# Kernel optimization log

Hardware: AMD Instinct MI355X
Metric: run time of the kernel (lower is better)

Reference implementation:

```python
import jax, jax.numpy as jnp
import numpy as np

B, S, D_IN, D = 8, 8192, 512, 512  # batch, seq_len, input_dim, dim (dim_inner = dim since expansion=1.0)


def log_g(x):
    # log-space version of g(x) = relu(x)+0.5 for x>=0, sigmoid(x) for x<0
    return jnp.where(x >= 0, jnp.log(jax.nn.relu(x) + 0.5), -jax.nn.softplus(-x))


def heinsen_scan_log(log_coeffs, log_values):
    # parallel linear-recurrence solve in log space
    a_star = jnp.cumsum(log_coeffs, axis=1)                       # [B, S+1, D]
    log_h = a_star + jax.lax.cumlogsumexp(log_values - a_star, axis=1)
    return jnp.exp(log_h)


def setup_inputs() -> dict:
    key = jax.random.key(0)
    k1, k2, k3 = jax.random.split(key, 3)
    x = jax.random.normal(k1, (B, S, D_IN), dtype=jnp.float32)
    prev_hidden = jax.random.normal(k2, (B, D), dtype=jnp.float32)
    W = jax.random.normal(k3, (D_IN, 2 * D), dtype=jnp.float32) / np.sqrt(D_IN)
    return {"x": x, "prev_hidden": prev_hidden, "W": W}


def reference(x, prev_hidden, W):
    seq_len = x.shape[1]
    hidden_gate = jnp.einsum('bsi,id->bsd', x, W)                 # [B, S, 2D]
    hidden, gate = jnp.split(hidden_gate, 2, axis=-1)             # [B, S, D] each
    log_coeffs = -jax.nn.softplus(gate)                           # log(1 - z)
    log_z = -jax.nn.softplus(-gate)                               # log(z)
    log_values = log_z + log_g(hidden)                            # log(z * h_tilde)
    # prepend previous hidden state as step 0 of the recurrence
    log_values = jnp.concatenate([log_g(prev_hidden)[:, None, :], log_values], axis=1)  # [B, S+1, D]
    log_coeffs = jnp.pad(log_coeffs, ((0, 0), (1, 0), (0, 0)))     # [B, S+1, D]
    h = heinsen_scan_log(log_coeffs, log_values)                  # [B, S+1, D]
    out = h[:, -seq_len:]                                         # [B, S, D]
    return out  # to_out is identity since expansion_factor == 1.0
```

## Files before the change

### kernel.cpp

```cpp
#include <hip/hip_runtime.h>
#include <stdint.h>

#define Bb   8
#define Ss   8192
#define DIN  512
#define Dd   512
#define M_TOT (Bb * Ss)
#define NC   64
#define CL   128

static const size_t CV_OFF  = 0;
static const size_t XS_OFF  = 134217728ull;
static const size_t WT_OFF  = XS_OFF + 67108864ull;
static const size_t AG_OFF  = WT_OFF + 1048576ull;
static const size_t HIN_OFF = AG_OFF + 2097152ull;
static const size_t WS_NEED = HIN_OFF + 1048576ull;

typedef short  short8 __attribute__((ext_vector_type(8)));
typedef float  f32x4  __attribute__((ext_vector_type(4)));

__device__ __forceinline__ unsigned short bf16_rne(float f) {
  uint32_t u = __float_as_uint(f);
  u += 0x7fffu + ((u >> 16) & 1u);
  return (unsigned short)(u >> 16);
}

__device__ __forceinline__ void gload16(const unsigned short* g, void* l) {
  __builtin_amdgcn_global_load_lds(
      (const __attribute__((address_space(1))) uint32_t*)g,
      (__attribute__((address_space(3))) uint32_t*)l, 16, 0, 0);
}

__global__ void k_prep(const float* __restrict__ x, const float* __restrict__ W,
                       unsigned short* __restrict__ xs, unsigned short* __restrict__ wt) {
  const int bx = blockIdx.x;
  if (bx < 4096) {
    const size_t n4 = (size_t)M_TOT * DIN / 4;
    for (size_t i = (size_t)bx * 256 + threadIdx.x; i < n4; i += (size_t)4096 * 256) {
      float4 v = ((const float4*)x)[i];
      size_t e = i * 4;
      size_t r = e >> 9;
      int    k = (int)(e & 511);
      ushort4 hi;
      unsigned short* hp = (unsigned short*)&hi;
      hp[0] = bf16_rne(v.x); hp[1] = bf16_rne(v.y);
      hp[2] = bf16_rne(v.z); hp[3] = bf16_rne(v.w);
      *(ushort4*)(xs + r * 512 + k) = hi;
    }
  } else {
    const int t0 = (bx - 4096) * 256 + threadIdx.x;
    for (int i = t0; i < 1024 * 512; i += 131072) {
      int n = i >> 9;
      int k = i & 511;
      int t = n >> 5, u = n & 31;
      int j = 16 * t + (u & 15) + ((u & 16) ? 512 : 0);
      wt[i] = bf16_rne(W[(size_t)k * 1024 + j]);
    }
  }
}

__global__ void __launch_bounds__(256) k_gemm(const unsigned short* __restrict__ xs,
                                              const unsigned short* __restrict__ wt,
                                              uint32_t* __restrict__ cvu,
                                              float2* __restrict__ agg) {
  __shared__ __align__(16) unsigned short As[2][128 * 32];
  __shared__ __align__(16) unsigned short Bsh[2][128 * 32];
  __shared__ float aggC[2][2][2][16];
  __shared__ float aggV[2][2][2][16];

  const int tid  = threadIdx.x;
  const int lane = tid & 63;
  const int wave = tid >> 6;
  const int wr = wave >> 1, wc = wave & 1;

  const int bid = blockIdx.x;
  const int xcd = bid & 7;
  const int j8  = bid >> 3;
  const int mb  = xcd * 64 + (j8 >> 3);
  const int nb  = j8 & 7;
  const int m0 = mb * 128, n0 = nb * 128;

  f32x4 acc[4][4] = {};

  const int trow = tid >> 2;
  const int tks  = 8 * ((tid & 3) ^ ((tid >> 3) & 3));
  const size_t aoff0 = (size_t)(m0 + trow) * 512 + tks;
  const size_t aoff1 = aoff0 + (size_t)64 * 512;
  const size_t boff0 = (size_t)(n0 + trow) * 512 + tks;
  const size_t boff1 = boff0 + (size_t)64 * 512;

  const int ra = (lane & 15) * 32 + 8 * ((lane >> 4) ^ ((lane >> 1) & 3));

#define STAGE(bf, k0) { \
    char* la = (char*)As  + (bf) * 8192 + wave * 1024; \
    char* lb = (char*)Bsh + (bf) * 8192 + wave * 1024; \
    gload16(xs + aoff0 + (k0), la); \
    gload16(xs + aoff1 + (k0), la + 4096); \
    gload16(wt + boff0 + (k0), lb); \
    gload16(wt + boff1 + (k0), lb + 4096); }

#define COMPUTE(bf) { \
    const unsigned short* Ab = &As[bf][0]; \
    const unsigned short* Bb2 = &Bsh[bf][0]; \
    short8 af[4], bfr[4]; \
    _Pragma("unroll") for (int m = 0; m < 4; ++m) \
      af[m] = *(const short8*)(Ab + (wr * 64 + 16 * m) * 32 + ra); \
    _Pragma("unroll") for (int n = 0; n < 4; ++n) \
      bfr[n] = *(const short8*)(Bb2 + (wc * 64 + 16 * n) * 32 + ra); \
    _Pragma("unroll") for (int m = 0; m < 4; ++m) \
      _Pragma("unroll") for (int n = 0; n < 4; ++n) \
        acc[m][n] = __builtin_amdgcn_mfma_f32_16x16x32_bf16(af[m], bfr[n], acc[m][n], 0, 0, 0); }

  STAGE(0, 0);
  __syncthreads();
  int buf = 0;
  for (int kt = 0; kt < 15; ++kt) {
    STAGE(buf ^ 1, (kt + 1) * 32);
    COMPUTE(buf);
    __syncthreads();
    buf ^= 1;
  }
  COMPUTE(buf);

  const int q     = lane >> 4;
  const int rbase = m0 + wr * 64 + (q << 2);
  const int dbase = nb * 64 + wc * 32 + (lane & 15);

  float CW[2] = {1.f, 1.f};
  float VW[2] = {0.f, 0.f};

#pragma unroll
  for (int m = 0; m < 4; ++m) {
#pragma unroll
    for (int t = 0; t < 2; ++t) {
      float cseg = 1.f, vseg = 0.f;
#pragma unroll
      for (int j = 0; j < 4; ++j) {
        float hid = acc[m][2 * t][j];
        float gat = acc[m][2 * t + 1][j];
        float eg = __expf(gat);
        float c  = 1.f / (1.f + eg);
        float z  = 1.f - c;
        float gv = (hid >= 0.f) ? (hid + 0.5f) : (1.f / (1.f + __expf(-hid)));
        float v  = z * gv;
        int R = rbase + 16 * m + j;
        int d = dbase + 16 * t;
        cvu[(size_t)R * 512 + d] =
            (uint32_t)bf16_rne(c) | ((uint32_t)bf16_rne(v) << 16);
        vseg = fmaf(c, vseg, v);
        cseg *= c;
      }
      {
        float Cp = __shfl_xor(cseg, 16);
        float Vp = __shfl_xor(vseg, 16);
        if (q & 1) { vseg = fmaf(cseg, Vp, vseg); cseg = Cp * cseg; }
        else       { vseg = fmaf(Cp, vseg, Vp);   cseg = cseg * Cp; }
        Cp = __shfl_xor(cseg, 32);
        Vp = __shfl_xor(vseg, 32);
        if (q & 2) { vseg = fmaf(cseg, Vp, vseg); cseg = Cp * cseg; }
        else       { vseg = fmaf(Cp, vseg, Vp);   cseg = cseg * Cp; }
      }
      VW[t] = fmaf(cseg, VW[t], vseg);
      CW[t] *= cseg;
    }
  }

  if (lane < 16) {
#pragma unroll
    for (int t = 0; t < 2; ++t) {
      aggC[wr][wc][t][lane] = CW[t];
      aggV[wr][wc][t][lane] = VW[t];
    }
  }
  __syncthreads();
  if (wr == 0 && lane < 16) {
#pragma unroll
    for (int t = 0; t < 2; ++t) {
      float C1 = aggC[1][wc][t][lane];
      float V1 = aggV[1][wc][t][lane];
      int d = nb * 64 + wc * 32 + t * 16 + lane;
      agg[(size_t)mb * 512 + d] = make_float2(CW[t] * C1, fmaf(C1, VW[t], V1));
    }
  }
}

__global__ void k_chain(const float* __restrict__ prev, const float2* __restrict__ agg,
                        float* __restrict__ hin) {
  const int b = blockIdx.x >> 1;
  const int d = (blockIdx.x & 1) * 256 + threadIdx.x;
  float p = prev[b * 512 + d];
  float h = (p >= 0.f) ? (p + 0.5f) : (1.f / (1.f + __expf(-p)));
  float2 a[NC];
#pragma unroll
  for (int k = 0; k < NC; ++k)
    a[k] = agg[((size_t)(b * NC + k)) * 512 + d];
#pragma unroll
  for (int k = 0; k < NC; ++k) {
    hin[((size_t)(b * NC + k)) * 512 + d] = h;
    h = fmaf(a[k].x, h, a[k].y);
  }
}

__global__ void k_scan_out(const uint32_t* __restrict__ cvu, const float* __restrict__ hin,
                           float* __restrict__ out) {
  const int bid = blockIdx.x;
  const int chunk = bid & 63;
  const int b = bid >> 6;
  const int d0 = threadIdx.x * 2;
  float2 h2 = *(const float2*)(hin + ((size_t)(b * NC + chunk)) * 512 + d0);
  const size_t base = ((size_t)(b * Ss + chunk * CL)) * 512 + d0;
#pragma unroll 8
  for (int i = 0; i < CL; ++i) {
    uint2 t = *(const uint2*)(cvu + base + (size_t)i * 512);
    float c0 = __uint_as_float(t.x << 16);
    float v0 = __uint_as_float(t.x & 0xFFFF0000u);
    float c1 = __uint_as_float(t.y << 16);
    float v1 = __uint_as_float(t.y & 0xFFFF0000u);
    h2.x = fmaf(c0, h2.x, v0);
    h2.y = fmaf(c1, h2.y, v1);
    *(float2*)(out + base + (size_t)i * 512) = h2;
  }
}

extern "C" void kernel_launch(void* const* d_in, const int* in_sizes, int n_in,
                              void* d_out, int out_size, void* d_ws, size_t ws_size,
                              hipStream_t stream) {
  if (ws_size < WS_NEED) return;

  const float* x    = (const float*)d_in[0];
  const float* prev = (const float*)d_in[1];
  const float* W    = (const float*)d_in[2];
  float* out = (float*)d_out;
  char* ws = (char*)d_ws;

  uint32_t*       cvu = (uint32_t*)(ws + CV_OFF);
  unsigned short* xs  = (unsigned short*)(ws + XS_OFF);
  unsigned short* wt  = (unsigned short*)(ws + WT_OFF);
  float2*         agg = (float2*)(ws + AG_OFF);
  float*          hin = (float*)(ws + HIN_OFF);

  k_prep<<<dim3(4608), dim3(256), 0, stream>>>(x, W, xs, wt);
  k_gemm<<<dim3(4096), dim3(256), 0, stream>>>(xs, wt, cvu, agg);
  k_chain<<<dim3(16), dim3(256), 0, stream>>>(prev, agg, hin);
  k_scan_out<<<dim3(512), dim3(256), 0, stream>>>(cvu, hin, out);
}
```

Before: 377.1 us.

## Enlarge GEMM M-tile to 256 rows and coalesce the W transpose reads

The fused GEMM+gate kernel now computes a 256x128 output tile per block, with each wave holding 8x4 MFMA accumulators, which halves the grid and doubles A-operand reuse per B load. Each wave writes its own 128-row chunk aggregate directly, so the shared-memory cross-wave combine and its barrier are gone. The chunk indexing stays consistent with the 64 chunks of 128 rows used by the chain and scan kernels. The W conversion in the prep kernel now reads W contiguously and scatters the writes instead of gathering strided reads. The risks are more register pressure (launch bounds set to 2 blocks), lower occupancy, and fewer blocks to balance across CUs.

```diff
diff --git a/kernel.cpp b/kernel.cpp
--- a/kernel.cpp
+++ b/kernel.cpp
@@ -49,24 +49,23 @@
     }
   } else {
     const int t0 = (bx - 4096) * 256 + threadIdx.x;
-    for (int i = t0; i < 1024 * 512; i += 131072) {
-      int n = i >> 9;
-      int k = i & 511;
-      int t = n >> 5, u = n & 31;
-      int j = 16 * t + (u & 15) + ((u & 16) ? 512 : 0);
-      wt[i] = bf16_rne(W[(size_t)k * 1024 + j]);
-    }
-  }
-}
-
-__global__ void __launch_bounds__(256) k_gemm(const unsigned short* __restrict__ xs,
-                                              const unsigned short* __restrict__ wt,
-                                              uint32_t* __restrict__ cvu,
-                                              float2* __restrict__ agg) {
-  __shared__ __align__(16) unsigned short As[2][128 * 32];
+    for (int i = t0; i < 512 * 1024; i += 131072) {
+      int k = i >> 10;
+      int j = i & 1023;
+      float w = W[i];
+      int n = (j < 512) ? (32 * (j >> 4) + (j & 15))
+                        : (32 * ((j - 512) >> 4) + 16 + ((j - 512) & 15));
+      wt[n * 512 + k] = bf16_rne(w);
+    }
+  }
+}
+
+__global__ void __launch_bounds__(256, 2) k_gemm(const unsigned short* __restrict__ xs,
+                                                 const unsigned short* __restrict__ wt,
+                                                 uint32_t* __restrict__ cvu,
+                                                 float2* __restrict__ agg) {
+  __shared__ __align__(16) unsigned short As[2][256 * 32];
   __shared__ __align__(16) unsigned short Bsh[2][128 * 32];
-  __shared__ float aggC[2][2][2][16];
-  __shared__ float aggV[2][2][2][16];
 
   const int tid  = threadIdx.x;
   const int lane = tid & 63;
@@ -76,38 +75,42 @@
   const int bid = blockIdx.x;
   const int xcd = bid & 7;
   const int j8  = bid >> 3;
-  const int mb  = xcd * 64 + (j8 >> 3);
+  const int mb  = xcd * 32 + (j8 >> 3);
   const int nb  = j8 & 7;
-  const int m0 = mb * 128, n0 = nb * 128;
-
-  f32x4 acc[4][4] = {};
+  const int m0 = mb * 256, n0 = nb * 128;
+
+  f32x4 acc[8][4] = {};
 
   const int trow = tid >> 2;
   const int tks  = 8 * ((tid & 3) ^ ((tid >> 3) & 3));
   const size_t aoff0 = (size_t)(m0 + trow) * 512 + tks;
   const size_t aoff1 = aoff0 + (size_t)64 * 512;
+  const size_t aoff2 = aoff0 + (size_t)128 * 512;
+  const size_t aoff3 = aoff0 + (size_t)192 * 512;
   const size_t boff0 = (size_t)(n0 + trow) * 512 + tks;
   const size_t boff1 = boff0 + (size_t)64 * 512;
 
   const int ra = (lane & 15) * 32 + 8 * ((lane >> 4) ^ ((lane >> 1) & 3));
 
 #define STAGE(bf, k0) { \
-    char* la = (char*)As  + (bf) * 8192 + wave * 1024; \
-    char* lb = (char*)Bsh + (bf) * 8192 + wave * 1024; \
+    char* la = (char*)As  + (bf) * 16384 + wave * 1024; \
+    char* lb = (char*)Bsh + (bf) * 8192  + wave * 1024; \
     gload16(xs + aoff0 + (k0), la); \
     gload16(xs + aoff1 + (k0), la + 4096); \
+    gload16(xs + aoff2 + (k0), la + 8192); \
+    gload16(xs + aoff3 + (k0), la + 12288); \
     gload16(wt + boff0 + (k0), lb); \
     gload16(wt + boff1 + (k0), lb + 4096); }
 
 #define COMPUTE(bf) { \
-    const unsigned short* Ab = &As[bf][0]; \
+    const unsigned short* Ab  = &As[bf][0]; \
     const unsigned short* Bb2 = &Bsh[bf][0]; \
-    short8 af[4], bfr[4]; \
-    _Pragma("unroll") for (int m = 0; m < 4; ++m) \
-      af[m] = *(const short8*)(Ab + (wr * 64 + 16 * m) * 32 + ra); \
+    short8 af[8], bfr[4]; \
+    _Pragma("unroll") for (int m = 0; m < 8; ++m) \
+      af[m] = *(const short8*)(Ab + (wr * 128 + 16 * m) * 32 + ra); \
     _Pragma("unroll") for (int n = 0; n < 4; ++n) \
       bfr[n] = *(const short8*)(Bb2 + (wc * 64 + 16 * n) * 32 + ra); \
-    _Pragma("unroll") for (int m = 0; m < 4; ++m) \
+    _Pragma("unroll") for (int m = 0; m < 8; ++m) \
       _Pragma("unroll") for (int n = 0; n < 4; ++n) \
         acc[m][n] = __builtin_amdgcn_mfma_f32_16x16x32_bf16(af[m], bfr[n], acc[m][n], 0, 0, 0); }
 
@@ -123,14 +126,15 @@
   COMPUTE(buf);
 
   const int q     = lane >> 4;
-  const int rbase = m0 + wr * 64 + (q << 2);
+  const int rbase = m0 + wr * 128 + (q << 2);
   const int dbase = nb * 64 + wc * 32 + (lane & 15);
+  const int cg    = 2 * mb + wr;
 
   float CW[2] = {1.f, 1.f};
   float VW[2] = {0.f, 0.f};
 
 #pragma unroll
-  for (int m = 0; m < 4; ++m) {
+  for (int m = 0; m < 8; ++m) {
 #pragma unroll
     for (int t = 0; t < 2; ++t) {
       float cseg = 1.f, vseg = 0.f;
@@ -168,18 +172,8 @@
   if (lane < 16) {
 #pragma unroll
     for (int t = 0; t < 2; ++t) {
-      aggC[wr][wc][t][lane] = CW[t];
-      aggV[wr][wc][t][lane] = VW[t];
-    }
-  }
-  __syncthreads();
-  if (wr == 0 && lane < 16) {
-#pragma unroll
-    for (int t = 0; t < 2; ++t) {
-      float C1 = aggC[1][wc][t][lane];
-      float V1 = aggV[1][wc][t][lane];
       int d = nb * 64 + wc * 32 + t * 16 + lane;
-      agg[(size_t)mb * 512 + d] = make_float2(CW[t] * C1, fmaf(C1, VW[t], V1));
+      agg[(size_t)cg * 512 + d] = make_float2(CW[t], VW[t]);
     }
   }
 }
@@ -240,7 +234,7 @@
   float*          hin = (float*)(ws + HIN_OFF);
 
   k_prep<<<dim3(4608), dim3(256), 0, stream>>>(x, W, xs, wt);
-  k_gemm<<<dim3(4096), dim3(256), 0, stream>>>(xs, wt, cvu, agg);
+  k_gemm<<<dim3(2048), dim3(256), 0, stream>>>(xs, wt, cvu, agg);
   k_chain<<<dim3(16), dim3(256), 0, stream>>>(prev, agg, hin);
   k_scan_out<<<dim3(512), dim3(256), 0, stream>>>(cvu, hin, out);
 }
```

Result: no change. 382.8 us (+1.5%).

## Fuse chunk-carry chain into scan kernel and use nontemporal scan I/O

Applied to the files above, without the earlier changes.

Drops the separate k_chain launch. Each scan block now recomputes its incoming hidden state by folding the per-chunk aggregates of all earlier chunks. The scan kernel moves to one element per thread over 1024 blocks and uses nontemporal loads and stores for the streamed cvu/out data. The W transpose in prep now reads W coalesced and scatters the writes. In exchange for removing a launch and a serialized tiny kernel, later chunks do redundant serial work of up to 63 aggregate steps.

```diff
diff --git a/kernel.cpp b/kernel.cpp
--- a/kernel.cpp
+++ b/kernel.cpp
@@ -13,8 +13,7 @@
 static const size_t XS_OFF  = 134217728ull;
 static const size_t WT_OFF  = XS_OFF + 67108864ull;
 static const size_t AG_OFF  = WT_OFF + 1048576ull;
-static const size_t HIN_OFF = AG_OFF + 2097152ull;
-static const size_t WS_NEED = HIN_OFF + 1048576ull;
+static const size_t WS_NEED = AG_OFF + 2097152ull;
 
 typedef short  short8 __attribute__((ext_vector_type(8)));
 typedef float  f32x4  __attribute__((ext_vector_type(4)));
@@ -49,12 +48,13 @@
     }
   } else {
     const int t0 = (bx - 4096) * 256 + threadIdx.x;
-    for (int i = t0; i < 1024 * 512; i += 131072) {
-      int n = i >> 9;
-      int k = i & 511;
-      int t = n >> 5, u = n & 31;
-      int j = 16 * t + (u & 15) + ((u & 16) ? 512 : 0);
-      wt[i] = bf16_rne(W[(size_t)k * 1024 + j]);
+    for (int i = t0; i < 512 * 1024; i += 131072) {
+      int k = i >> 10;
+      int j = i & 1023;
+      float w = W[i];
+      int n = (j < 512) ? (32 * (j >> 4) + (j & 15))
+                        : (32 * ((j - 512) >> 4) + 16 + ((j - 512) & 15));
+      wt[n * 512 + k] = bf16_rne(w);
     }
   }
 }
@@ -100,7 +100,7 @@
     gload16(wt + boff1 + (k0), lb + 4096); }
 
 #define COMPUTE(bf) { \
-    const unsigned short* Ab = &As[bf][0]; \
+    const unsigned short* Ab  = &As[bf][0]; \
     const unsigned short* Bb2 = &Bsh[bf][0]; \
     short8 af[4], bfr[4]; \
     _Pragma("unroll") for (int m = 0; m < 4; ++m) \
@@ -184,41 +184,34 @@
   }
 }
 
-__global__ void k_chain(const float* __restrict__ prev, const float2* __restrict__ agg,
-                        float* __restrict__ hin) {
-  const int b = blockIdx.x >> 1;
-  const int d = (blockIdx.x & 1) * 256 + threadIdx.x;
+__global__ void k_scan_out(const uint32_t* __restrict__ cvu,
+                           const float* __restrict__ prev,
+                           const float2* __restrict__ agg,
+                           float* __restrict__ out) {
+  const int bid   = blockIdx.x;
+  const int dh    = bid & 1;
+  const int chunk = (bid >> 1) & 63;
+  const int b     = bid >> 7;
+  const int d     = dh * 256 + threadIdx.x;
+
   float p = prev[b * 512 + d];
   float h = (p >= 0.f) ? (p + 0.5f) : (1.f / (1.f + __expf(-p)));
-  float2 a[NC];
-#pragma unroll
-  for (int k = 0; k < NC; ++k)
-    a[k] = agg[((size_t)(b * NC + k)) * 512 + d];
-#pragma unroll
-  for (int k = 0; k < NC; ++k) {
-    hin[((size_t)(b * NC + k)) * 512 + d] = h;
-    h = fmaf(a[k].x, h, a[k].y);
-  }
-}
-
-__global__ void k_scan_out(const uint32_t* __restrict__ cvu, const float* __restrict__ hin,
-                           float* __restrict__ out) {
-  const int bid = blockIdx.x;
-  const int chunk = bid & 63;
-  const int b = bid >> 6;
-  const int d0 = threadIdx.x * 2;
-  float2 h2 = *(const float2*)(hin + ((size_t)(b * NC + chunk)) * 512 + d0);
-  const size_t base = ((size_t)(b * Ss + chunk * CL)) * 512 + d0;
+
+  const float2* ag = agg + (size_t)(b * NC) * 512 + d;
+#pragma unroll 4
+  for (int k = 0; k < chunk; ++k) {
+    float2 a = ag[(size_t)k * 512];
+    h = fmaf(a.x, h, a.y);
+  }
+
+  const size_t base = ((size_t)(b * Ss + chunk * CL)) * 512 + d;
 #pragma unroll 8
   for (int i = 0; i < CL; ++i) {
-    uint2 t = *(const uint2*)(cvu + base + (size_t)i * 512);
-    float c0 = __uint_as_float(t.x << 16);
-    float v0 = __uint_as_float(t.x & 0xFFFF0000u);
-    float c1 = __uint_as_float(t.y << 16);
-    float v1 = __uint_as_float(t.y & 0xFFFF0000u);
-    h2.x = fmaf(c0, h2.x, v0);
-    h2.y = fmaf(c1, h2.y, v1);
-    *(float2*)(out + base + (size_t)i * 512) = h2;
+    uint32_t t = __builtin_nontemporal_load(cvu + base + (size_t)i * 512);
+    float c = __uint_as_float(t << 16);
+    float v = __uint_as_float(t & 0xFFFF0000u);
+    h = fmaf(c, h, v);
+    __builtin_nontemporal_store(h, out + base + (size_t)i * 512);
   }
 }
 
@@ -237,10 +230,8 @@
   unsigned short* xs  = (unsigned short*)(ws + XS_OFF);
   unsigned short* wt  = (unsigned short*)(ws + WT_OFF);
   float2*         agg = (float2*)(ws + AG_OFF);
-  float*          hin = (float*)(ws + HIN_OFF);
 
   k_prep<<<dim3(4608), dim3(256), 0, stream>>>(x, W, xs, wt);
   k_gemm<<<dim3(4096), dim3(256), 0, stream>>>(xs, wt, cvu, agg);
-  k_chain<<<dim3(16), dim3(256), 0, stream>>>(prev, agg, hin);
-  k_scan_out<<<dim3(512), dim3(256), 0, stream>>>(cvu, hin, out);
-}
+  k_scan_out<<<dim3(1024), dim3(256), 0, stream>>>(cvu, prev, agg, out);
+}
```

After: 367.6 us. 1.03x faster.
